# Optimization experiments

Measured on AMD Instinct MI355X. Metric: run time of the kernel, lower is better.

The kernel has to match this reference:

```python
import jax, jax.numpy as jnp
import numpy as np

N, G, K, D = 16, 4096, 8, 2  # agents, grid points (64x64 flattened), fiber dim, manifold dim


def setup_inputs() -> dict:
    key = jax.random.key(0)
    k0, k1, k2, k3 = jax.random.split(key, 4)
    I = jnp.eye(K, dtype=jnp.float32)
    # frames and links: identity + small perturbation (invertible, as init_twist_scale=0.05 implies)
    omega = I + 0.05 * jax.random.normal(k0, (N, G, K, K), dtype=jnp.float32)
    links = I + 0.05 * jax.random.normal(k1, (N, D, G, K, K), dtype=jnp.float32)
    mu_q = jax.random.normal(k2, (N, G, K), dtype=jnp.float32)
    A = 0.3 * jax.random.normal(k3, (N, G, K, K), dtype=jnp.float32)
    sigma_q = A @ A.swapaxes(-1, -2) + I  # SPD covariances
    return {"omega": omega, "links": links, "mu_q": mu_q, "sigma_q": sigma_q}


def reference(omega, links, mu_q, sigma_q):
    """pairwise_alignment_with_twists: E[i,j,g] = KL(q_i || Omega_ij[q_j]).

    full_transport: Omega_ij = omega_i @ V_i @ inv(omega_j),
    V_i = I + sum_d (link_{i,d} - I)   (links depend only on i, per source).
    """
    I = jnp.eye(K, dtype=omega.dtype)
    V = I + jnp.sum(links - I, axis=1)                       # (N,G,K,K)
    T = omega @ V                                            # omega_i V_i, (N,G,K,K)
    omega_inv = jnp.linalg.inv(omega)                        # (N,G,K,K)
    Om = jnp.einsum('igab,jgbc->ijgac', T, omega_inv)        # (N,N,G,K,K)

    mu_t = jnp.einsum('ijgab,jgb->ijga', Om, mu_q)           # transported means
    sig_t = jnp.einsum('ijgab,jgbc,ijgdc->ijgad', Om, sigma_q, Om)  # Om Sigma Om^T

    inv2 = jnp.linalg.inv(sig_t)                             # Sigma2^{-1}
    diff = mu_t - mu_q[:, None]                              # (N,N,G,K)
    tr = jnp.einsum('ijgab,igba->ijg', inv2, sigma_q)        # tr(Sigma2^{-1} Sigma1)
    quad = jnp.einsum('ijga,ijgab,ijgb->ijg', diff, inv2, diff)
    ld2 = jnp.linalg.slogdet(sig_t)[1]                       # (N,N,G)
    ld1 = jnp.linalg.slogdet(sigma_q)[1]                     # (N,G)
    E = 0.5 * (tr + quad - K + ld2 - ld1[:, None, :])
    # zero the diagonal (i == j skipped in the original loop)
    mask = 1.0 - jnp.eye(N, dtype=E.dtype)
    return E * mask[:, :, None]
```

## Files before the change

### kernel.cpp

```cpp
#include <hip/hip_runtime.h>
#include <math.h>

#define NN 16
#define GG 4096
#define STR 76
#define NWG GG

template <int CTRL>
__device__ __forceinline__ float dppf(float x) {
    return __builtin_bit_cast(float, __builtin_amdgcn_mov_dpp(
        __builtin_bit_cast(int, x), CTRL, 0xF, 0xF, true));
}
__device__ __forceinline__ float qb(float x, int L) {
    switch (L) {
        case 0:  return dppf<0x00>(x);
        case 1:  return dppf<0x55>(x);
        case 2:  return dppf<0xAA>(x);
        default: return dppf<0xFF>(x);
    }
}
__device__ __forceinline__ float qsum(float x) {
    x += dppf<0xB1>(x);
    x += dppf<0x4E>(x);
    return x;
}
__device__ __forceinline__ void bcast_row(float out[8], const float r0[8],
                                          const float r1[8], int k) {
#pragma unroll
    for (int c = 0; c < 8; ++c) {
        float s = (k < 4) ? r0[c] : r1[c];
        out[c] = qb(s, k & 3);
    }
}
__device__ __forceinline__ float sel_lo(const float r[8], int q) {
    return (q == 0) ? r[0] : (q == 1) ? r[1] : (q == 2) ? r[2] : r[3];
}
__device__ __forceinline__ float sel_hi(const float r[8], int q) {
    return (q == 0) ? r[4] : (q == 1) ? r[5] : (q == 2) ? r[6] : r[7];
}
__device__ __forceinline__ void ld_row(float r[8], const float* p) {
    float4 x = *(const float4*)p, y = *(const float4*)(p + 4);
    r[0] = x.x; r[1] = x.y; r[2] = x.z; r[3] = x.w;
    r[4] = y.x; r[5] = y.y; r[6] = y.z; r[7] = y.w;
}
__device__ __forceinline__ void st_row(float* p, const float r[8]) {
    *(float4*)p       = make_float4(r[0], r[1], r[2], r[3]);
    *(float4*)(p + 4) = make_float4(r[4], r[5], r[6], r[7]);
}
__device__ __forceinline__ float dot8(const float a[8], const float b[8]) {
    float s = a[0] * b[0];
    s = fmaf(a[1], b[1], s); s = fmaf(a[2], b[2], s);
    s = fmaf(a[3], b[3], s); s = fmaf(a[4], b[4], s);
    s = fmaf(a[5], b[5], s); s = fmaf(a[6], b[6], s);
    s = fmaf(a[7], b[7], s);
    return s;
}

__device__ __forceinline__ float gj4(float r0[8], float r1[8], int q) {
    float pp = 1.0f;
#pragma unroll
    for (int k = 0; k < 8; ++k) {
        float Mk[8];
        bcast_row(Mk, r0, r1, k);
        float p = Mk[k];
        pp *= p;
        float ip = 1.0f / p;
        bool own0 = (k < 4) && (q == k);
        bool own1 = (k >= 4) && (q == k - 4);
        float m0 = -(own0 ? -1.0f : r0[k]) * ip;
        float m1 = -(own1 ? -1.0f : r1[k]) * ip;
#pragma unroll
        for (int c = 0; c < 8; ++c) {
            float b0 = own0 ? 0.0f : r0[c];
            float b1 = own1 ? 0.0f : r1[c];
            r0[c] = fmaf(m0, Mk[c], b0);
            r1[c] = fmaf(m1, Mk[c], b1);
        }
        r0[k] = m0;
        r1[k] = m1;
    }
    return pp;
}

__global__ __launch_bounds__(64) void pairkl_kernel(
    const float* __restrict__ omega, const float* __restrict__ links,
    const float* __restrict__ mu, const float* __restrict__ sigma,
    float* __restrict__ out) {
    __shared__ __align__(16) float sh_x[NN][STR];
    __shared__ __align__(16) float sh_y[NN][STR];

    const int bid  = blockIdx.x;
    const int g    = (bid & 7) * (NWG / 8) + (bid >> 3);
    const int lane = threadIdx.x;
    const int item = lane >> 2;
    const int q    = lane & 3;
    const int mb   = (item * GG + g) * 64;

    float o0[8], o1[8], s0[8], s1[8], v0[8], v1[8], mq[8];
    {
        const float* l0p = links + ((item * 2 + 0) * GG + g) * 64;
        const float* l1p = links + ((item * 2 + 1) * GG + g) * 64;
        float la[8], lb[8];
        ld_row(la, l0p + q * 8);
        ld_row(lb, l1p + q * 8);
#pragma unroll
        for (int c = 0; c < 8; ++c) v0[c] = la[c] + lb[c] - ((c == q) ? 1.f : 0.f);
        ld_row(la, l0p + (q + 4) * 8);
        ld_row(lb, l1p + (q + 4) * 8);
#pragma unroll
        for (int c = 0; c < 8; ++c) v1[c] = la[c] + lb[c] - ((c == q + 4) ? 1.f : 0.f);
    }
    ld_row(o0, omega + mb + q * 8);
    ld_row(o1, omega + mb + (q + 4) * 8);
    ld_row(s0, sigma + mb + q * 8);
    ld_row(s1, sigma + mb + (q + 4) * 8);
    ld_row(mq, mu + (item * GG + g) * 8);

    float ldT, u_lo, u_hi, uf[8];
    {
        float R0[8], R1[8];
#pragma unroll
        for (int c = 0; c < 8; ++c) { R0[c] = 0.f; R1[c] = 0.f; }
#pragma unroll
        for (int b = 0; b < 8; ++b) {
            float Vb[8]; bcast_row(Vb, v0, v1, b);
#pragma unroll
            for (int c = 0; c < 8; ++c) {
                R0[c] = fmaf(o0[b], Vb[c], R0[c]);
                R1[c] = fmaf(o1[b], Vb[c], R1[c]);
            }
        }
        ldT = logf(fabsf(gj4(R0, R1, q)));
        float Z0[8], Z1[8];
#pragma unroll
        for (int c = 0; c < 8; ++c) { Z0[c] = 0.f; Z1[c] = 0.f; }
#pragma unroll
        for (int b = 0; b < 8; ++b) {
            float Sb[8]; bcast_row(Sb, s0, s1, b);
#pragma unroll
            for (int c = 0; c < 8; ++c) {
                Z0[c] = fmaf(R0[b], Sb[c], Z0[c]);
                Z1[c] = fmaf(R1[b], Sb[c], Z1[c]);
            }
        }
        u_lo = dot8(R0, mq);
        u_hi = dot8(R1, mq);
#pragma unroll
        for (int c = 0; c < 4; ++c) { uf[c] = qb(u_lo, c); uf[c + 4] = qb(u_hi, c); }
#pragma unroll
        for (int c = 0; c < 8; ++c) {
            float Wc[8]; bcast_row(Wc, R0, R1, c);
            v0[c] = fmaf(u_lo, uf[c], dot8(Z0, Wc));
            v1[c] = fmaf(u_hi, uf[c], dot8(Z1, Wc));
        }
        st_row(&sh_x[item][q * 8], v0);
        st_row(&sh_x[item][(q + 4) * 8], v1);
    }

    float ld1, cc, wf[8];
    {
        ld1 = logf(fabsf(gj4(s0, s1, q)));
        cc  = qsum(dot8(s0, mq) * sel_lo(mq, q) + dot8(s1, mq) * sel_hi(mq, q));
        float t10[8], t11[8];
#pragma unroll
        for (int c = 0; c < 8; ++c) { t10[c] = 0.f; t11[c] = 0.f; }
#pragma unroll
        for (int a = 0; a < 8; ++a) {
            float Oa[8]; bcast_row(Oa, o0, o1, a);
            float Sa[8]; bcast_row(Sa, s0, s1, a);
            float oqa = sel_lo(Oa, q), oqa4 = sel_hi(Oa, q);
#pragma unroll
            for (int c = 0; c < 8; ++c) {
                t10[c] = fmaf(oqa,  Sa[c], t10[c]);
                t11[c] = fmaf(oqa4, Sa[c], t11[c]);
            }
        }
        float w_lo = dot8(t10, mq), w_hi = dot8(t11, mq);
#pragma unroll
        for (int c = 0; c < 4; ++c) { wf[c] = qb(w_lo, c); wf[c + 4] = qb(w_hi, c); }
#pragma unroll
        for (int c = 0; c < 8; ++c) { s0[c] = 0.f; s1[c] = 0.f; }
#pragma unroll
        for (int b = 0; b < 8; ++b) {
            float Ob[8]; bcast_row(Ob, o0, o1, b);
#pragma unroll
            for (int c = 0; c < 8; ++c) {
                s0[c] = fmaf(t10[b], Ob[c], s0[c]);
                s1[c] = fmaf(t11[b], Ob[c], s1[c]);
            }
        }
        st_row(&sh_y[item][q * 8], s0);
        st_row(&sh_y[item][(q + 4) * 8], s1);
    }
    float ldo = logf(fabsf(gj4(o0, o1, q)));

    if (q == 0) {
        float a_i = 2.f * ldT - ld1;
        float s_j = ld1 - 2.f * ldo + cc - 8.0f;
        *(float4*)&sh_x[item][64] = make_float4(uf[0], uf[1], uf[2], uf[3]);
        *(float4*)&sh_x[item][68] = make_float4(uf[4], uf[5], uf[6], uf[7]);
        *(float4*)&sh_x[item][72] = make_float4(a_i, 1.f, 0.f, 0.f);
        *(float4*)&sh_y[item][64] =
            make_float4(-2.f * wf[0], -2.f * wf[1], -2.f * wf[2], -2.f * wf[3]);
        *(float4*)&sh_y[item][68] =
            make_float4(-2.f * wf[4], -2.f * wf[5], -2.f * wf[6], -2.f * wf[7]);
        *(float4*)&sh_y[item][72] = make_float4(1.f, s_j, 0.f, 0.f);
    }
    asm volatile("" ::: "memory");

    {
        const int i0 = lane >> 3, j0 = lane & 7;
        const int i1 = i0 + 8, j1 = j0 + 8;
        const float4* x0 = (const float4*)&sh_x[i0][0];
        const float4* x1 = (const float4*)&sh_x[i1][0];
        const float4* y0 = (const float4*)&sh_y[j0][0];
        const float4* y1 = (const float4*)&sh_y[j1][0];
        float d00 = 0.f, d01 = 0.f, d10 = 0.f, d11 = 0.f;
#pragma unroll
        for (int k = 0; k < STR / 4; ++k) {
            float4 a0 = x0[k], a1 = x1[k], b0 = y0[k], b1 = y1[k];
            d00 = fmaf(a0.x, b0.x, d00); d00 = fmaf(a0.y, b0.y, d00);
            d00 = fmaf(a0.z, b0.z, d00); d00 = fmaf(a0.w, b0.w, d00);
            d01 = fmaf(a0.x, b1.x, d01); d01 = fmaf(a0.y, b1.y, d01);
            d01 = fmaf(a0.z, b1.z, d01); d01 = fmaf(a0.w, b1.w, d01);
            d10 = fmaf(a1.x, b0.x, d10); d10 = fmaf(a1.y, b0.y, d10);
            d10 = fmaf(a1.z, b0.z, d10); d10 = fmaf(a1.w, b0.w, d10);
            d11 = fmaf(a1.x, b1.x, d11); d11 = fmaf(a1.y, b1.y, d11);
            d11 = fmaf(a1.z, b1.z, d11); d11 = fmaf(a1.w, b1.w, d11);
        }
        const bool dg = (i0 == j0);
        out[(i0 * NN + j0) * GG + g] = dg ? 0.f : 0.5f * d00;
        out[(i0 * NN + j1) * GG + g] = 0.5f * d01;
        out[(i1 * NN + j0) * GG + g] = 0.5f * d10;
        out[(i1 * NN + j1) * GG + g] = dg ? 0.f : 0.5f * d11;
    }
}

extern "C" void kernel_launch(void* const* d_in, const int* in_sizes, int n_in,
                              void* d_out, int out_size, void* d_ws, size_t ws_size,
                              hipStream_t stream) {
    const float* omega = (const float*)d_in[0];
    const float* links = (const float*)d_in[1];
    const float* mu    = (const float*)d_in[2];
    const float* sigma = (const float*)d_in[3];
    float* out = (float*)d_out;
    hipLaunchKernelGGL(pairkl_kernel, dim3(NWG), dim3(64), 0, stream,
                       omega, links, mu, sigma, out);
}
```

Before: 26.88 us.

## Stage sigma in LDS, derive log-det of omega from T and V

Sigma rows are staged in shared memory instead of registers, which cuts live register pressure, and are reloaded when needed. The Gauss-Jordan determinant of omega is replaced by a cheaper forward-only LU determinant of V, with log|omega| taken as log|T| - log|V|. The omega^T Sigma omega product is reorganised to use column loads of omega from global memory and wave reductions for w. A hazard is that the staged sigma region aliases sh_y, which is overwritten later, and nothing visible synchronises the reads against that write.

```diff
diff --git a/kernel.cpp b/kernel.cpp
--- a/kernel.cpp
+++ b/kernel.cpp
@@ -4,6 +4,7 @@
 #define NN 16
 #define GG 4096
 #define STR 76
+#define SSTR 68
 #define NWG GG
 
 template <int CTRL>
@@ -82,12 +83,37 @@
     return pp;
 }
 
+__device__ __forceinline__ float ludet4(float r0[8], float r1[8], int q) {
+    float pp = 1.0f;
+#pragma unroll
+    for (int k = 0; k < 8; ++k) {
+        float Mk[8];
+#pragma unroll
+        for (int c = k; c < 8; ++c) {
+            float s = (k < 4) ? r0[c] : r1[c];
+            Mk[c] = qb(s, k & 3);
+        }
+        float p = Mk[k];
+        pp *= p;
+        float ip = 1.0f / p;
+        float f0 = (q > k) ? r0[k] * ip : 0.f;
+        float f1 = (q + 4 > k) ? r1[k] * ip : 0.f;
+#pragma unroll
+        for (int c = k + 1; c < 8; ++c) {
+            r0[c] = fmaf(-f0, Mk[c], r0[c]);
+            r1[c] = fmaf(-f1, Mk[c], r1[c]);
+        }
+    }
+    return pp;
+}
+
 __global__ __launch_bounds__(64) void pairkl_kernel(
     const float* __restrict__ omega, const float* __restrict__ links,
     const float* __restrict__ mu, const float* __restrict__ sigma,
     float* __restrict__ out) {
     __shared__ __align__(16) float sh_x[NN][STR];
     __shared__ __align__(16) float sh_y[NN][STR];
+    float* sh_s = &sh_y[0][0];
 
     const int bid  = blockIdx.x;
     const int g    = (bid & 7) * (NWG / 8) + (bid >> 3);
@@ -96,7 +122,7 @@
     const int q    = lane & 3;
     const int mb   = (item * GG + g) * 64;
 
-    float o0[8], o1[8], s0[8], s1[8], v0[8], v1[8], mq[8];
+    float v0[8], v1[8], o0[8], o1[8], mq[8];
     {
         const float* l0p = links + ((item * 2 + 0) * GG + g) * 64;
         const float* l1p = links + ((item * 2 + 1) * GG + g) * 64;
@@ -112,89 +138,97 @@
     }
     ld_row(o0, omega + mb + q * 8);
     ld_row(o1, omega + mb + (q + 4) * 8);
-    ld_row(s0, sigma + mb + q * 8);
-    ld_row(s1, sigma + mb + (q + 4) * 8);
+    {
+        float sa[8], sb[8];
+        ld_row(sa, sigma + mb + q * 8);
+        ld_row(sb, sigma + mb + (q + 4) * 8);
+        st_row(&sh_s[item * SSTR + q * 8], sa);
+        st_row(&sh_s[item * SSTR + (q + 4) * 8], sb);
+    }
     ld_row(mq, mu + (item * GG + g) * 8);
 
-    float ldT, u_lo, u_hi, uf[8];
-    {
-        float R0[8], R1[8];
-#pragma unroll
-        for (int c = 0; c < 8; ++c) { R0[c] = 0.f; R1[c] = 0.f; }
-#pragma unroll
-        for (int b = 0; b < 8; ++b) {
-            float Vb[8]; bcast_row(Vb, v0, v1, b);
-#pragma unroll
-            for (int c = 0; c < 8; ++c) {
-                R0[c] = fmaf(o0[b], Vb[c], R0[c]);
-                R1[c] = fmaf(o1[b], Vb[c], R1[c]);
-            }
-        }
-        ldT = logf(fabsf(gj4(R0, R1, q)));
-        float Z0[8], Z1[8];
-#pragma unroll
-        for (int c = 0; c < 8; ++c) { Z0[c] = 0.f; Z1[c] = 0.f; }
-#pragma unroll
-        for (int b = 0; b < 8; ++b) {
-            float Sb[8]; bcast_row(Sb, s0, s1, b);
-#pragma unroll
-            for (int c = 0; c < 8; ++c) {
-                Z0[c] = fmaf(R0[b], Sb[c], Z0[c]);
-                Z1[c] = fmaf(R1[b], Sb[c], Z1[c]);
-            }
-        }
-        u_lo = dot8(R0, mq);
-        u_hi = dot8(R1, mq);
-#pragma unroll
-        for (int c = 0; c < 4; ++c) { uf[c] = qb(u_lo, c); uf[c + 4] = qb(u_hi, c); }
-#pragma unroll
-        for (int c = 0; c < 8; ++c) {
-            float Wc[8]; bcast_row(Wc, R0, R1, c);
-            v0[c] = fmaf(u_lo, uf[c], dot8(Z0, Wc));
-            v1[c] = fmaf(u_hi, uf[c], dot8(Z1, Wc));
-        }
-        st_row(&sh_x[item][q * 8], v0);
-        st_row(&sh_x[item][(q + 4) * 8], v1);
-    }
-
-    float ld1, cc, wf[8];
-    {
-        ld1 = logf(fabsf(gj4(s0, s1, q)));
-        cc  = qsum(dot8(s0, mq) * sel_lo(mq, q) + dot8(s1, mq) * sel_hi(mq, q));
-        float t10[8], t11[8];
-#pragma unroll
-        for (int c = 0; c < 8; ++c) { t10[c] = 0.f; t11[c] = 0.f; }
-#pragma unroll
-        for (int a = 0; a < 8; ++a) {
-            float Oa[8]; bcast_row(Oa, o0, o1, a);
-            float Sa[8]; bcast_row(Sa, s0, s1, a);
-            float oqa = sel_lo(Oa, q), oqa4 = sel_hi(Oa, q);
-#pragma unroll
-            for (int c = 0; c < 8; ++c) {
-                t10[c] = fmaf(oqa,  Sa[c], t10[c]);
-                t11[c] = fmaf(oqa4, Sa[c], t11[c]);
-            }
-        }
-        float w_lo = dot8(t10, mq), w_hi = dot8(t11, mq);
-#pragma unroll
-        for (int c = 0; c < 4; ++c) { wf[c] = qb(w_lo, c); wf[c + 4] = qb(w_hi, c); }
-#pragma unroll
-        for (int c = 0; c < 8; ++c) { s0[c] = 0.f; s1[c] = 0.f; }
-#pragma unroll
-        for (int b = 0; b < 8; ++b) {
-            float Ob[8]; bcast_row(Ob, o0, o1, b);
-#pragma unroll
-            for (int c = 0; c < 8; ++c) {
-                s0[c] = fmaf(t10[b], Ob[c], s0[c]);
-                s1[c] = fmaf(t11[b], Ob[c], s1[c]);
-            }
-        }
-        st_row(&sh_y[item][q * 8], s0);
-        st_row(&sh_y[item][(q + 4) * 8], s1);
-    }
-    float ldo = logf(fabsf(gj4(o0, o1, q)));
+    float R0[8], R1[8];
+#pragma unroll
+    for (int c = 0; c < 8; ++c) { R0[c] = 0.f; R1[c] = 0.f; }
+#pragma unroll
+    for (int b = 0; b < 8; ++b) {
+        float Vb[8]; bcast_row(Vb, v0, v1, b);
+#pragma unroll
+        for (int c = 0; c < 8; ++c) {
+            R0[c] = fmaf(o0[b], Vb[c], R0[c]);
+            R1[c] = fmaf(o1[b], Vb[c], R1[c]);
+        }
+    }
+    float ldV = logf(fabsf(ludet4(v0, v1, q)));
+    float ldT = logf(fabsf(gj4(R0, R1, q)));
+    float Z0[8], Z1[8];
+#pragma unroll
+    for (int c = 0; c < 8; ++c) { Z0[c] = 0.f; Z1[c] = 0.f; }
+#pragma unroll
+    for (int b = 0; b < 8; ++b) {
+        float sr[8]; ld_row(sr, &sh_s[item * SSTR + b * 8]);
+#pragma unroll
+        for (int c = 0; c < 8; ++c) {
+            Z0[c] = fmaf(R0[b], sr[c], Z0[c]);
+            Z1[c] = fmaf(R1[b], sr[c], Z1[c]);
+        }
+    }
+    float u_lo = dot8(R0, mq), u_hi = dot8(R1, mq);
+    float uf[8];
+#pragma unroll
+    for (int c = 0; c < 4; ++c) { uf[c] = qb(u_lo, c); uf[c + 4] = qb(u_hi, c); }
+#pragma unroll
+    for (int c = 0; c < 8; ++c) {
+        float Wc[8]; bcast_row(Wc, R0, R1, c);
+        v0[c] = fmaf(u_lo, uf[c], dot8(Z0, Wc));
+        v1[c] = fmaf(u_hi, uf[c], dot8(Z1, Wc));
+    }
+    st_row(&sh_x[item][q * 8], v0);
+    st_row(&sh_x[item][(q + 4) * 8], v1);
+
+    float s0[8], s1[8];
+    ld_row(s0, &sh_s[item * SSTR + q * 8]);
+    ld_row(s1, &sh_s[item * SSTR + (q + 4) * 8]);
+    float ld1 = logf(fabsf(gj4(s0, s1, q)));
+    float mql = sel_lo(mq, q), mqh = sel_hi(mq, q);
+    float cc  = qsum(dot8(s0, mq) * mql + dot8(s1, mq) * mqh);
+    float U0[8], U1[8];
+#pragma unroll
+    for (int c = 0; c < 8; ++c) { U0[c] = 0.f; U1[c] = 0.f; }
+#pragma unroll
+    for (int b = 0; b < 8; ++b) {
+        float Ob[8]; bcast_row(Ob, o0, o1, b);
+#pragma unroll
+        for (int c = 0; c < 8; ++c) {
+            U0[c] = fmaf(s0[b], Ob[c], U0[c]);
+            U1[c] = fmaf(s1[b], Ob[c], U1[c]);
+        }
+    }
+    float wf[8];
+#pragma unroll
+    for (int c = 0; c < 8; ++c) wf[c] = qsum(fmaf(mql, U0[c], mqh * U1[c]));
+    float oc0[8], oc1[8];
+#pragma unroll
+    for (int a = 0; a < 8; ++a) {
+        oc0[a] = omega[mb + a * 8 + q];
+        oc1[a] = omega[mb + a * 8 + q + 4];
+    }
+#pragma unroll
+    for (int c = 0; c < 8; ++c) { s0[c] = 0.f; s1[c] = 0.f; }
+#pragma unroll
+    for (int a = 0; a < 8; ++a) {
+        float Ua[8]; bcast_row(Ua, U0, U1, a);
+#pragma unroll
+        for (int c = 0; c < 8; ++c) {
+            s0[c] = fmaf(oc0[a], Ua[c], s0[c]);
+            s1[c] = fmaf(oc1[a], Ua[c], s1[c]);
+        }
+    }
+    st_row(&sh_y[item][q * 8], s0);
+    st_row(&sh_y[item][(q + 4) * 8], s1);
 
     if (q == 0) {
+        float ldo = ldT - ldV;
         float a_i = 2.f * ldT - ld1;
         float s_j = ld1 - 2.f * ldo + cc - 8.0f;
         *(float4*)&sh_x[item][64] = make_float4(uf[0], uf[1], uf[2], uf[3]);
```

New measurement: 27.65 us. 2.9% more time.
